# Optimization experiments

Measured on AMD Instinct MI355X. Metric: run time of the kernel, lower is better.

The kernel has to match this reference:

```python
import jax, jax.numpy as jnp
import numpy as np

N_ATOMS = 500_000
N_EDGES = 1_000_000
N_BLOCKS = 100_000
HIDDEN = 128
ATOM_VOCAB = 128
BOND_VOCAB = 5


def setup_inputs() -> dict:
    key = jax.random.key(0)
    ks = jax.random.split(key, 12)
    A = jax.random.randint(ks[0], (N_ATOMS,), 0, ATOM_VOCAB)
    src = jax.random.randint(ks[1], (N_EDGES,), 0, N_ATOMS)
    dst = jax.random.randint(ks[2], (N_EDGES,), 0, N_ATOMS)
    btype = jax.random.randint(ks[3], (N_EDGES,), 0, BOND_VOCAB)
    bonds = jnp.stack([src, dst, btype], axis=1)  # [E, 3]
    # monotone atom -> block assignment (like length_to_batch_id)
    block_ids = jnp.sort(jax.random.randint(ks[4], (N_ATOMS,), 0, N_BLOCKS))
    generate_mask = jax.random.bernoulli(ks[5], 0.5, (N_BLOCKS,))
    s = 0.02
    atom_table = jax.random.normal(ks[6], (ATOM_VOCAB, HIDDEN), jnp.float32) * s
    bond_table = jax.random.normal(ks[7], (BOND_VOCAB, HIDDEN), jnp.float32) * s
    eps = jnp.zeros((), jnp.float32)  # GINE epsilon
    W1 = jax.random.normal(ks[8], (HIDDEN, HIDDEN), jnp.float32) * s
    b1 = jnp.zeros((HIDDEN,), jnp.float32)
    W2 = jax.random.normal(ks[9], (HIDDEN, HIDDEN), jnp.float32) * s
    b2 = jnp.zeros((HIDDEN,), jnp.float32)
    return {"A": A, "bonds": bonds, "block_ids": block_ids,
            "generate_mask": generate_mask, "atom_table": atom_table,
            "bond_table": bond_table, "eps": eps,
            "W1": W1, "b1": b1, "W2": W2, "b2": b2}


def reference(A, bonds, block_ids, generate_mask, atom_table, bond_table,
              eps, W1, b1, W2, b2):
    n_atoms = A.shape[0]
    n_blocks = generate_mask.shape[0]
    # context mask per atom; edges kept only if both endpoints are context
    ctx = ~generate_mask[block_ids]                      # [N] bool
    src, dst, btype = bonds[:, 0], bonds[:, 1], bonds[:, 2]
    edge_keep = (ctx[src] & ctx[dst]).astype(atom_table.dtype)[:, None]  # [E,1]
    # embedding gathers
    H = atom_table[A]                                    # [N, D]
    e_attr = bond_table[btype]                           # [E, D]
    # GINEConv: h_i' = MLP((1+eps)*h_i + sum_{j->i} relu(h_j + e_ji))
    # masked edges contribute zero (equivalent to filtering them out)
    msg = jax.nn.relu(H[src] + e_attr) * edge_keep       # [E, D]
    agg = jax.ops.segment_sum(msg, dst, num_segments=n_atoms)  # [N, D]
    h = (1.0 + eps) * H + agg
    h = jax.nn.relu(h @ W1 + b1) @ W2 + b2               # [N, D]
    # std-conserving scatter mean over blocks: sum / sqrt(count)
    blk_sum = jax.ops.segment_sum(h, block_ids, num_segments=n_blocks)  # [B, D]
    cnt = jax.ops.segment_sum(jnp.ones((n_atoms,), h.dtype), block_ids,
                              num_segments=n_blocks)     # [B]
    topo = blk_sum / jnp.sqrt(jnp.maximum(cnt, 1.0))[:, None]
    # zero out the generated (masked) blocks
    topo = jnp.where(generate_mask[:, None], jnp.zeros_like(topo), topo)
    return topo
```

## Files before the change

### kernel.cpp

```cpp
#include <hip/hip_runtime.h>
#include <math.h>

#define NA 500000
#define NE 1000000
#define NB 100000
#define HID 128
#define NCHUNK 489
#define NT 7813
#define NBT 1563
#define NAC 272000
#define CAPA 14
#define SST 132
#define HSB 136

typedef __attribute__((ext_vector_type(8))) short bf16x8;
typedef __attribute__((ext_vector_type(4))) float f32x4;

static __device__ __forceinline__ unsigned short bf1(float a) {
    unsigned ua = __float_as_uint(a);
    ua += 0x7fffu + ((ua >> 16) & 1u);
    return (unsigned short)(ua >> 16);
}
static __device__ __forceinline__ unsigned bfpack(float a, float b) {
    unsigned ua = __float_as_uint(a); ua += 0x7fffu + ((ua >> 16) & 1u);
    unsigned ub = __float_as_uint(b); ub += 0x7fffu + ((ub >> 16) & 1u);
    return (ua >> 16) | (ub & 0xffff0000u);
}
static __device__ __forceinline__ float bff(unsigned short h) {
    return __uint_as_float((unsigned)h << 16);
}

__global__ __launch_bounds__(256) void k_scanprep(
    const int* __restrict__ block_ids, const int* __restrict__ gmask,
    int* __restrict__ cnt, int* __restrict__ acp, int* __restrict__ totB,
    const float* __restrict__ at, const float* __restrict__ bt,
    const float* __restrict__ W1, const float* __restrict__ W2,
    const float* __restrict__ b1, const float* __restrict__ epsp,
    float* __restrict__ TAW, float* __restrict__ MTW,
    unsigned short* __restrict__ wt2)
{
    __shared__ float smem[17920];
    const int blk = blockIdx.x;
    const int tid = threadIdx.x;

    if (blk < NCHUNK) {
        int* sd = (int*)smem;
        int base = blk * 1024 + tid * 4;
        int c0 = 0, c1 = 0, c2 = 0, c3 = 0;
        if (base < NA) {
            int4 b = *(const int4*)(block_ids + base);
            atomicAdd(&cnt[b.x], 1); atomicAdd(&cnt[b.y], 1);
            atomicAdd(&cnt[b.z], 1); atomicAdd(&cnt[b.w], 1);
            c0 = (gmask[b.x] == 0); c1 = (gmask[b.y] == 0);
            c2 = (gmask[b.z] == 0); c3 = (gmask[b.w] == 0);
        }
        int s = c0 + c1 + c2 + c3;
        sd[tid] = s;
        __syncthreads();
        for (int o = 1; o < 256; o <<= 1) {
            int x = (tid >= o) ? sd[tid - o] : 0;
            __syncthreads();
            sd[tid] += x;
            __syncthreads();
        }
        int run = sd[tid] - s;
        if (tid == 255) totB[blk] = sd[255];
        if (base < NA) {
            acp[base + 0] = c0 ? run : -1; run += c0;
            acp[base + 1] = c1 ? run : -1; run += c1;
            acp[base + 2] = c2 ? run : -1; run += c2;
            acp[base + 3] = c3 ? run : -1;
        }
    } else if (blk < NCHUNK + 64) {
        const int blk2 = blk - NCHUNK;
        float* sW1 = smem;
        float (*sIn)[HID] = (float(*)[HID])(smem + 16384);
        for (int i = tid; i < HID * HID / 4; i += 256)
            ((float4*)sW1)[i] = ((const float4*)W1)[i];
        for (int x = tid; x < 12 * HID; x += 256) {
            int rr = x >> 7, k = x & 127;
            int r = blk2 * 12 + rr;
            float v = 0.f;
            if (r < 128) v = at[r * HID + k];
            else {
                int m = r - 128;
                int a = m / 5, bb = m - a * 5;
                v = fmaxf(at[a * HID + k] + bt[bb * HID + k], 0.f);
            }
            sIn[rr][k] = v;
        }
        __syncthreads();
        float ope = 1.0f + epsp[0];
        for (int x = tid; x < 12 * HID; x += 256) {
            int rr = x >> 7, c = x & 127;
            int r = blk2 * 12 + rr;
            float acc = 0.f;
#pragma unroll 8
            for (int k = 0; k < HID; ++k)
                acc = fmaf(sIn[rr][k], sW1[k * HID + c], acc);
            if (r < 128) TAW[r * HID + c] = ope * acc + b1[c];
            else         MTW[(r - 128) * HID + c] = acc;
        }
    } else {
        int id = (blk - NCHUNK - 64) * 256 + tid;
        int n = id >> 7, k = id & 127;
        wt2[id] = bf1(W2[k * HID + n]);
    }
}

__global__ __launch_bounds__(256) void k_finc(int* __restrict__ acp,
                                              const int* __restrict__ totB,
                                              const int* __restrict__ A,
                                              const int* __restrict__ block_ids,
                                              int* __restrict__ catomA,
                                              int* __restrict__ nctxp) {
    __shared__ int sT[512];
    __shared__ int sS[256];
    const int t = threadIdx.x;
    int a0 = (2 * t     < NCHUNK) ? totB[2 * t]     : 0;
    int a1 = (2 * t + 1 < NCHUNK) ? totB[2 * t + 1] : 0;
    int s = a0 + a1;
    sS[t] = s;
    __syncthreads();
    for (int o = 1; o < 256; o <<= 1) {
        int x = (t >= o) ? sS[t - o] : 0;
        __syncthreads();
        sS[t] += x;
        __syncthreads();
    }
    int run = sS[t] - s;
    sT[2 * t] = run;
    sT[2 * t + 1] = run + a0;
    if (blockIdx.x == 0 && t == 255) nctxp[0] = sS[255];
    __syncthreads();

    int i = blockIdx.x * 256 + t;
    if (i < NA) {
        int v = acp[i];
        if (v >= 0) {
            int p = v + sT[i >> 10];
            int a = A[i];
            acp[i] = (p << 7) | a;
            catomA[p] = (block_ids[i] << 7) | a;
        }
    }
}

__global__ __launch_bounds__(256) void k_escatter(const int* __restrict__ bonds,
                                                  const int* __restrict__ acp,
                                                  int* __restrict__ adeg,
                                                  unsigned short* __restrict__ buf2) {
    int e4 = blockIdx.x * 256 + threadIdx.x;
    if (e4 >= NE / 4) return;
    const int4* b4 = (const int4*)bonds;
    int4 q0 = b4[e4 * 3 + 0];
    int4 q1 = b4[e4 * 3 + 1];
    int4 q2 = b4[e4 * 3 + 2];
    int ss[4] = {q0.x, q0.w, q1.z, q2.y};
    int dd[4] = {q0.y, q1.x, q1.w, q2.z};
    int tt[4] = {q0.z, q1.y, q2.x, q2.w};
#pragma unroll
    for (int k = 0; k < 4; ++k) {
        int va = acp[ss[k]];
        int vd = acp[dd[k]];
        if ((va | vd) >= 0) {
            int pd = vd >> 7;
            int slot = atomicAdd(&adeg[pd], 1);
            if (slot < CAPA)
                buf2[(size_t)pd * CAPA + slot] =
                    (unsigned short)((va & 127) * 5 + tt[k]);
        }
    }
}

__global__ __launch_bounds__(256, 8) void k_h1(
    const int* __restrict__ catomA, const int* __restrict__ nctxp,
    const int* __restrict__ adeg, const unsigned short* __restrict__ buf2,
    const float* __restrict__ TAW, const float* __restrict__ MTW,
    float* __restrict__ out)
{
    __shared__ unsigned short sH[64 * HSB];
    __shared__ int sAid[64];
    __shared__ int sBid[64];
    __shared__ int sDeg[64];

    const int nctx = nctxp[0];
    const int base = blockIdx.x * 64;
    if (base >= nctx) return;
    const int tid = threadIdx.x;

    if (tid < 64) {
        int idx = base + tid;
        if (idx < nctx) {
            int ca = catomA[idx];
            sAid[tid] = ca & 127;
            sBid[tid] = ca >> 7;
            int d = adeg[idx];
            sDeg[tid] = d < CAPA ? d : CAPA;
        } else {
            sAid[tid] = -1; sBid[tid] = -1; sDeg[tid] = 0;
        }
    }
    __syncthreads();

    {
        const int al = tid >> 2;
        const int ks = (tid & 3) * 32;
        const int aid = sAid[al];
        float hacc[32];
#pragma unroll
        for (int j = 0; j < 32; ++j) hacc[j] = 0.f;
        if (aid >= 0) {
            const int deg = sDeg[al];
            const unsigned* ep32 = (const unsigned*)(buf2 + (size_t)(base + al) * CAPA);
            unsigned ev[7];
#pragma unroll
            for (int j = 0; j < 7; ++j)
                if (2 * j < deg) ev[j] = ep32[j];
            const float4* tp = (const float4*)(TAW + aid * HID + ks);
#pragma unroll
            for (int j = 0; j < 8; ++j) {
                float4 v = tp[j];
                hacc[4 * j + 0] = v.x; hacc[4 * j + 1] = v.y;
                hacc[4 * j + 2] = v.z; hacc[4 * j + 3] = v.w;
            }
#pragma unroll
            for (int j = 0; j < 7; ++j) {
                if (2 * j < deg) {
                    const float4* mp = (const float4*)(MTW + (int)(ev[j] & 0xffffu) * HID + ks);
#pragma unroll
                    for (int q = 0; q < 8; ++q) {
                        float4 x = mp[q];
                        hacc[4 * q + 0] += x.x; hacc[4 * q + 1] += x.y;
                        hacc[4 * q + 2] += x.z; hacc[4 * q + 3] += x.w;
                    }
                }
                if (2 * j + 1 < deg) {
                    const float4* mp = (const float4*)(MTW + (int)(ev[j] >> 16) * HID + ks);
#pragma unroll
                    for (int q = 0; q < 8; ++q) {
                        float4 x = mp[q];
                        hacc[4 * q + 0] += x.x; hacc[4 * q + 1] += x.y;
                        hacc[4 * q + 2] += x.z; hacc[4 * q + 3] += x.w;
                    }
                }
            }
        }
        unsigned short* rp = sH + al * HSB + ks;
#pragma unroll
        for (int j = 0; j < 4; ++j) {
            uint4 u;
            u.x = bfpack(fmaxf(hacc[8 * j + 0], 0.f), fmaxf(hacc[8 * j + 1], 0.f));
            u.y = bfpack(fmaxf(hacc[8 * j + 2], 0.f), fmaxf(hacc[8 * j + 3], 0.f));
            u.z = bfpack(fmaxf(hacc[8 * j + 4], 0.f), fmaxf(hacc[8 * j + 5], 0.f));
            u.w = bfpack(fmaxf(hacc[8 * j + 6], 0.f), fmaxf(hacc[8 * j + 7], 0.f));
            *(uint4*)(rp + 8 * j) = u;
        }
    }
    __syncthreads();

    {
        int c = tid & 127;
        int r0 = (tid >> 7) * 32;
        float run = 0.f;
        int curb = sBid[r0];
        bool unsafe = (r0 == 0) ? true : (sBid[31] == curb);
        for (int r = r0; r < r0 + 32; ++r) {
            int b = sBid[r];
            if (b != curb) {
                if (curb >= 0) {
                    float* o = out + (size_t)curb * HID + c;
                    if (unsafe) atomicAdd(o, run); else *o = run;
                }
                run = 0.f; curb = b; unsafe = false;
            }
            run += bff(sH[r * HSB + c]);
        }
        if (curb >= 0) {
            bool endUnsafe = (r0 == 0) ? (sBid[32] == curb) : true;
            float* o = out + (size_t)curb * HID + c;
            if (unsafe || endUnsafe) atomicAdd(o, run); else *o = run;
        }
    }
}

__global__ __launch_bounds__(256, 4) void k_gemm2(
    const unsigned short* __restrict__ wt2, const float* __restrict__ b2,
    const int* __restrict__ cnt, const int* __restrict__ gmask,
    float* __restrict__ out)
{
    __shared__ char lds[64 * SST * 4];
    __shared__ float sCnt[64];
    __shared__ float sScale[64];
    const int base = blockIdx.x * 64;
    const int tid = threadIdx.x;

    if (tid < 64) {
        int rb = base + tid;
        float cf = 0.f, sc = 0.f;
        if (rb < NB) {
            int c = cnt[rb];
            cf = (float)c;
            sc = (gmask[rb] == 0) ? rsqrtf((float)(c < 1 ? 1 : c)) : 0.f;
        }
        sCnt[tid] = cf;
        sScale[tid] = sc;
    }

    {
        const int al = tid >> 2;
        const int ks4 = tid & 3;
        const int rb = base + al;
        float v[32];
        if (rb < NB && gmask[rb] == 0) {
            const float4* sp = (const float4*)(out + (size_t)rb * HID + ks4 * 32);
#pragma unroll
            for (int j = 0; j < 8; ++j) {
                float4 x = sp[j];
                v[4 * j + 0] = x.x; v[4 * j + 1] = x.y;
                v[4 * j + 2] = x.z; v[4 * j + 3] = x.w;
            }
        } else {
#pragma unroll
            for (int j = 0; j < 32; ++j) v[j] = 0.f;
        }
        char* rowp = lds + al * 256;
#pragma unroll
        for (int c = 0; c < 4; ++c) {
            uint4 u;
            u.x = bfpack(v[8 * c + 0], v[8 * c + 1]);
            u.y = bfpack(v[8 * c + 2], v[8 * c + 3]);
            u.z = bfpack(v[8 * c + 4], v[8 * c + 5]);
            u.w = bfpack(v[8 * c + 6], v[8 * c + 7]);
            int chunk = (ks4 * 4 + c) ^ (al & 7);
            *(uint4*)(rowp + chunk * 16) = u;
        }
    }
    __syncthreads();

    const int w = tid >> 6;
    const int lane = tid & 63;
    const int rA = w * 16 + (lane & 15);
    const int g4 = lane >> 4;
    const int colb = lane & 15;

    f32x4 acc[8];
    {
        bf16x8 af[4];
#pragma unroll
        for (int k4 = 0; k4 < 4; ++k4) {
            int chunk = (k4 * 4 + g4) ^ (rA & 7);
            af[k4] = *(const bf16x8*)(lds + rA * 256 + chunk * 16);
        }
#pragma unroll
        for (int ct = 0; ct < 8; ++ct) {
            f32x4 a = {0.f, 0.f, 0.f, 0.f};
            const unsigned short* wp = wt2 + (ct * 16 + colb) * HID + g4 * 8;
#pragma unroll
            for (int k4 = 0; k4 < 4; ++k4) {
                bf16x8 bfr = *(const bf16x8*)(wp + k4 * 32);
                a = __builtin_amdgcn_mfma_f32_16x16x32_bf16(af[k4], bfr, a, 0, 0, 0);
            }
            acc[ct] = a;
        }
    }
    __syncthreads();

    float* sF = (float*)lds;
#pragma unroll
    for (int ct = 0; ct < 8; ++ct) {
        int col = ct * 16 + colb;
        float bv = b2[col];
#pragma unroll
        for (int r = 0; r < 4; ++r) {
            int row = w * 16 + g4 * 4 + r;
            sF[row * SST + col] = (acc[ct][r] + sCnt[row] * bv) * sScale[row];
        }
    }
    __syncthreads();

    {
        const int al = tid >> 2;
        const int ks = (tid & 3) * 32;
        const int rb = base + al;
        if (rb < NB && sScale[al] > 0.f) {
            float4* o = (float4*)(out + (size_t)rb * HID + ks);
            const float* rp = sF + al * SST + ks;
#pragma unroll
            for (int j = 0; j < 8; ++j) o[j] = *(const float4*)(rp + 4 * j);
        }
    }
}

extern "C" void kernel_launch(void* const* d_in, const int* in_sizes, int n_in,
                              void* d_out, int out_size, void* d_ws, size_t ws_size,
                              hipStream_t stream) {
    const int* A          = (const int*)d_in[0];
    const int* bonds      = (const int*)d_in[1];
    const int* block_ids  = (const int*)d_in[2];
    const int* gmask      = (const int*)d_in[3];
    const float* atom_table = (const float*)d_in[4];
    const float* bond_table = (const float*)d_in[5];
    const float* eps      = (const float*)d_in[6];
    const float* W1       = (const float*)d_in[7];
    const float* b1       = (const float*)d_in[8];
    const float* W2       = (const float*)d_in[9];
    const float* b2       = (const float*)d_in[10];
    float* out = (float*)d_out;
    char* ws = (char*)d_ws;

    int* cnt    = (int*)(ws + 0);
    int* adeg   = (int*)(ws + 400000);
    int* totB   = (int*)(ws + 1488000);
    int* nctx   = (int*)(ws + 1490000);
    float* TAW  = (float*)(ws + 1490048);
    float* MTW  = (float*)(ws + 1555584);
    unsigned short* wt2 = (unsigned short*)(ws + 1883264);
    int* acp    = (int*)(ws + 1916032);
    int* catomA = (int*)(ws + 3916032);
    unsigned short* buf2 = (unsigned short*)(ws + 5004032);

    hipMemsetAsync(cnt, 0, 1488000, stream);
    hipMemsetAsync(out, 0, (size_t)NB * HID * 4, stream);

    k_scanprep<<<NCHUNK + 128, 256, 0, stream>>>(
        block_ids, gmask, cnt, acp, totB,
        atom_table, bond_table, W1, W2, b1, eps, TAW, MTW, wt2);
    k_finc<<<(NA + 255) / 256, 256, 0, stream>>>(acp, totB, A, block_ids, catomA, nctx);
    k_escatter<<<(NE / 4 + 255) / 256, 256, 0, stream>>>(bonds, acp, adeg, buf2);
    k_h1<<<NT, 256, 0, stream>>>(catomA, nctx, adeg, buf2, TAW, MTW, out);
    k_gemm2<<<NBT, 256, 0, stream>>>(wt2, b2, cnt, gmask, out);
}
```

Baseline: 152.4 us.

## Fuse compaction finalize with edge scatter and replace full output memset

Folds the atom type into the local-scan position in the prep kernel, then merges the compaction-finalize and edge-scatter kernels into one launch. Edge blocks add the per-chunk global offset on the fly instead of waiting for a separate pass. Instead of memsetting the whole output, only block rows touched by context atoms are zeroed, by atoms at tile boundaries. The final GEMM now writes every row unconditionally and skips reading rows with zero count. This removes one launch and a large memset, but relies on subtle ordering between the zeroing and the scatter into out, with redundant prefix scans per block.

```diff
diff --git a/kernel.cpp b/kernel.cpp
--- a/kernel.cpp
+++ b/kernel.cpp
@@ -12,6 +12,8 @@
 #define CAPA 14
 #define SST 132
 #define HSB 136
+#define NEB 977
+#define NAB 1954
 
 typedef __attribute__((ext_vector_type(8))) short bf16x8;
 typedef __attribute__((ext_vector_type(4))) float f32x4;
@@ -32,6 +34,7 @@
 
 __global__ __launch_bounds__(256) void k_scanprep(
     const int* __restrict__ block_ids, const int* __restrict__ gmask,
+    const int* __restrict__ A,
     int* __restrict__ cnt, int* __restrict__ acp, int* __restrict__ totB,
     const float* __restrict__ at, const float* __restrict__ bt,
     const float* __restrict__ W1, const float* __restrict__ W2,
@@ -47,8 +50,10 @@
         int* sd = (int*)smem;
         int base = blk * 1024 + tid * 4;
         int c0 = 0, c1 = 0, c2 = 0, c3 = 0;
+        int4 av = make_int4(0, 0, 0, 0);
         if (base < NA) {
             int4 b = *(const int4*)(block_ids + base);
+            av = *(const int4*)(A + base);
             atomicAdd(&cnt[b.x], 1); atomicAdd(&cnt[b.y], 1);
             atomicAdd(&cnt[b.z], 1); atomicAdd(&cnt[b.w], 1);
             c0 = (gmask[b.x] == 0); c1 = (gmask[b.y] == 0);
@@ -66,10 +71,10 @@
         int run = sd[tid] - s;
         if (tid == 255) totB[blk] = sd[255];
         if (base < NA) {
-            acp[base + 0] = c0 ? run : -1; run += c0;
-            acp[base + 1] = c1 ? run : -1; run += c1;
-            acp[base + 2] = c2 ? run : -1; run += c2;
-            acp[base + 3] = c3 ? run : -1;
+            acp[base + 0] = c0 ? ((run << 7) | av.x) : -1; run += c0;
+            acp[base + 1] = c1 ? ((run << 7) | av.y) : -1; run += c1;
+            acp[base + 2] = c2 ? ((run << 7) | av.z) : -1; run += c2;
+            acp[base + 3] = c3 ? ((run << 7) | av.w) : -1;
         }
     } else if (blk < NCHUNK + 64) {
         const int blk2 = blk - NCHUNK;
@@ -108,12 +113,13 @@
     }
 }
 
-__global__ __launch_bounds__(256) void k_finc(int* __restrict__ acp,
-                                              const int* __restrict__ totB,
-                                              const int* __restrict__ A,
-                                              const int* __restrict__ block_ids,
-                                              int* __restrict__ catomA,
-                                              int* __restrict__ nctxp) {
+__global__ __launch_bounds__(256) void k_escfat(
+    const int* __restrict__ bonds, const int* __restrict__ acp,
+    const int* __restrict__ totB, const int* __restrict__ block_ids,
+    int* __restrict__ adeg, unsigned short* __restrict__ buf2,
+    int* __restrict__ catomA, int* __restrict__ nctxp,
+    float* __restrict__ out)
+{
     __shared__ int sT[512];
     __shared__ int sS[256];
     const int t = threadIdx.x;
@@ -134,41 +140,44 @@
     if (blockIdx.x == 0 && t == 255) nctxp[0] = sS[255];
     __syncthreads();
 
-    int i = blockIdx.x * 256 + t;
-    if (i < NA) {
-        int v = acp[i];
-        if (v >= 0) {
-            int p = v + sT[i >> 10];
-            int a = A[i];
-            acp[i] = (p << 7) | a;
-            catomA[p] = (block_ids[i] << 7) | a;
-        }
-    }
-}
-
-__global__ __launch_bounds__(256) void k_escatter(const int* __restrict__ bonds,
-                                                  const int* __restrict__ acp,
-                                                  int* __restrict__ adeg,
-                                                  unsigned short* __restrict__ buf2) {
-    int e4 = blockIdx.x * 256 + threadIdx.x;
-    if (e4 >= NE / 4) return;
-    const int4* b4 = (const int4*)bonds;
-    int4 q0 = b4[e4 * 3 + 0];
-    int4 q1 = b4[e4 * 3 + 1];
-    int4 q2 = b4[e4 * 3 + 2];
-    int ss[4] = {q0.x, q0.w, q1.z, q2.y};
-    int dd[4] = {q0.y, q1.x, q1.w, q2.z};
-    int tt[4] = {q0.z, q1.y, q2.x, q2.w};
-#pragma unroll
-    for (int k = 0; k < 4; ++k) {
-        int va = acp[ss[k]];
-        int vd = acp[dd[k]];
-        if ((va | vd) >= 0) {
-            int pd = vd >> 7;
-            int slot = atomicAdd(&adeg[pd], 1);
-            if (slot < CAPA)
-                buf2[(size_t)pd * CAPA + slot] =
-                    (unsigned short)((va & 127) * 5 + tt[k]);
+    if (blockIdx.x < NEB) {
+        int e4 = blockIdx.x * 256 + t;
+        if (e4 >= NE / 4) return;
+        const int4* b4 = (const int4*)bonds;
+        int4 q0 = b4[e4 * 3 + 0];
+        int4 q1 = b4[e4 * 3 + 1];
+        int4 q2 = b4[e4 * 3 + 2];
+        int ss[4] = {q0.x, q0.w, q1.z, q2.y};
+        int dd[4] = {q0.y, q1.x, q1.w, q2.z};
+        int tt[4] = {q0.z, q1.y, q2.x, q2.w};
+#pragma unroll
+        for (int k = 0; k < 4; ++k) {
+            int va = acp[ss[k]];
+            int vd = acp[dd[k]];
+            if ((va | vd) >= 0) {
+                int pd = (vd >> 7) + sT[dd[k] >> 10];
+                int slot = atomicAdd(&adeg[pd], 1);
+                if (slot < CAPA)
+                    buf2[(size_t)pd * CAPA + slot] =
+                        (unsigned short)((va & 127) * 5 + tt[k]);
+            }
+        }
+    } else {
+        int i = (blockIdx.x - NEB) * 256 + t;
+        if (i < NA) {
+            int v = acp[i];
+            if (v >= 0) {
+                int p = (v >> 7) + sT[i >> 10];
+                int bid = block_ids[i];
+                catomA[p] = (bid << 7) | (v & 127);
+                int pm = p & 31;
+                if (pm == 0 || pm == 31) {
+                    float4 z = make_float4(0.f, 0.f, 0.f, 0.f);
+                    float4* o = (float4*)(out + (size_t)bid * HID);
+#pragma unroll
+                    for (int j = 0; j < 32; ++j) o[j] = z;
+                }
+            }
         }
     }
 }
@@ -206,7 +215,7 @@
     {
         const int al = tid >> 2;
         const int ks = (tid & 3) * 32;
-        const int aid = sAid[al];
+        const int aid = (base + tid / 4 < nctx) ? sAid[al] : -1;
         float hacc[32];
 #pragma unroll
         for (int j = 0; j < 32; ++j) hacc[j] = 0.f;
@@ -312,7 +321,7 @@
         const int ks4 = tid & 3;
         const int rb = base + al;
         float v[32];
-        if (rb < NB && gmask[rb] == 0) {
+        if (rb < NB && gmask[rb] == 0 && cnt[rb] > 0) {
             const float4* sp = (const float4*)(out + (size_t)rb * HID + ks4 * 32);
 #pragma unroll
             for (int j = 0; j < 8; ++j) {
@@ -383,7 +392,7 @@
         const int al = tid >> 2;
         const int ks = (tid & 3) * 32;
         const int rb = base + al;
-        if (rb < NB && sScale[al] > 0.f) {
+        if (rb < NB) {
             float4* o = (float4*)(out + (size_t)rb * HID + ks);
             const float* rp = sF + al * SST + ks;
 #pragma unroll
@@ -421,13 +430,12 @@
     unsigned short* buf2 = (unsigned short*)(ws + 5004032);
 
     hipMemsetAsync(cnt, 0, 1488000, stream);
-    hipMemsetAsync(out, 0, (size_t)NB * HID * 4, stream);
 
     k_scanprep<<<NCHUNK + 128, 256, 0, stream>>>(
-        block_ids, gmask, cnt, acp, totB,
+        block_ids, gmask, A, cnt, acp, totB,
         atom_table, bond_table, W1, W2, b1, eps, TAW, MTW, wt2);
-    k_finc<<<(NA + 255) / 256, 256, 0, stream>>>(acp, totB, A, block_ids, catomA, nctx);
-    k_escatter<<<(NE / 4 + 255) / 256, 256, 0, stream>>>(bonds, acp, adeg, buf2);
+    k_escfat<<<NEB + NAB, 256, 0, stream>>>(
+        bonds, acp, totB, block_ids, adeg, buf2, catomA, nctx, out);
     k_h1<<<NT, 256, 0, stream>>>(catomA, nctx, adeg, buf2, TAW, MTW, out);
     k_gemm2<<<NBT, 256, 0, stream>>>(wt2, b2, cnt, gmask, out);
 }
```

Result: no change. 151.0 us (-0.9%).
